# Optimization experiments

Hardware: AMD Instinct MI355X
Metric: run time of the kernel (lower is better)

The kernel has to match this reference:

```python
import jax, jax.numpy as jnp
import numpy as np

N_NODES = 100000
N_EDGES = 6400000
NODE_IN = 128
HID = 64


def _mlp(x, w1, b1, w2, b2):
    # Linear -> ReLU -> Linear -> ReLU
    return jax.nn.relu(jax.nn.relu(x @ w1 + b1) @ w2 + b2)


def _edge_softmax_agg(node_h, logits, src, dst, n):
    # DGL edge_softmax: softmax of edge logits over incoming edges per dst node,
    # then weighted sum of src node features scattered to dst.
    m = jax.lax.stop_gradient(jax.ops.segment_max(logits, dst, num_segments=n))
    e = jnp.exp(logits - m[dst])
    s = jax.ops.segment_sum(e, dst, num_segments=n)
    w = e / s[dst]
    return jax.ops.segment_sum(w * node_h[src], dst, num_segments=n)


def setup_inputs() -> dict:
    key = jax.random.key(0)
    ks = jax.random.split(key, 24)
    d = {
        "node_feat": jax.random.normal(ks[0], (N_NODES, NODE_IN), jnp.float32),
        "edge_feat": jax.random.normal(ks[1], (N_EDGES, 1), jnp.float32),
        "edge_dist": jax.random.normal(ks[2], (N_EDGES, 1), jnp.float32),
        "src": jax.random.randint(ks[3], (N_EDGES,), 0, N_NODES, jnp.int32),
        "dst": jax.random.randint(ks[4], (N_EDGES,), 0, N_NODES, jnp.int32),
    }
    def lin(k, fin, fout):
        kw, kb = jax.random.split(k)
        return (jax.random.normal(kw, (fin, fout), jnp.float32) / np.sqrt(fin),
                jax.random.normal(kb, (fout,), jnp.float32) * 0.01)
    d["enc_w1"], d["enc_b1"] = lin(ks[5], NODE_IN, HID)
    d["enc_w2"], d["enc_b2"] = lin(ks[6], HID, 1)
    d["nu_w1"], d["nu_b1"] = lin(ks[7], 2, HID)
    d["nu_w2"], d["nu_b2"] = lin(ks[8], HID, 1)
    d["eu_w1"], d["eu_b1"] = lin(ks[9], 3, HID)
    d["eu_w2"], d["eu_b2"] = lin(ks[10], HID, 1)
    d["dec_w1"], d["dec_b1"] = lin(ks[11], 1, HID)
    d["dec_w2"], d["dec_b2"] = lin(ks[12], HID, 1)
    return d


def reference(node_feat, edge_feat, edge_dist, src, dst,
              enc_w1, enc_b1, enc_w2, enc_b2,
              nu_w1, nu_b1, nu_w2, nu_b2,
              eu_w1, eu_b1, eu_w2, eu_b2,
              dec_w1, dec_b1, dec_w2, dec_b2):
    n = node_feat.shape[0]
    # encoder on raw node features -> [N,1]
    h = _mlp(node_feat, enc_w1, enc_b1, enc_w2, enc_b2)
    # softmax aggregation weighted by edge 'dist'
    h = _edge_softmax_agg(h, edge_dist, src, dst, n)
    # edge update: concat([edge_feat, src_h, dst_h]) -> MLP -> [E,1]
    eh = _mlp(jnp.concatenate([edge_feat, h[src], h[dst]], axis=-1),
              eu_w1, eu_b1, eu_w2, eu_b2)
    # pull: sum incoming updated edge features per dst node
    agg = jax.ops.segment_sum(eh, dst, num_segments=n)
    # node update: concat([agg_m, h]) -> MLP -> [N,1]
    h = _mlp(jnp.concatenate([agg, h], axis=-1), nu_w1, nu_b1, nu_w2, nu_b2)
    # second softmax aggregation with updated edge features as logits
    h2 = _edge_softmax_agg(h, eh, src, dst, n)
    # decoder -> [N,1]
    return _mlp(h2, dec_w1, dec_b1, dec_w2, dec_b2)
```

## Files before the change

### kernel.cpp

```cpp
#include <hip/hip_runtime.h>


#define NHB 256

typedef int   iv4 __attribute__((ext_vector_type(4)));
typedef float fv4 __attribute__((ext_vector_type(4)));
typedef float fv2 __attribute__((ext_vector_type(2)));

#if __has_builtin(__builtin_elementwise_fma)
#define FMA2(a, b, c) __builtin_elementwise_fma((a), (b), (c))
#else
static __device__ __forceinline__ fv2 FMA2(fv2 a, fv2 b, fv2 c) {
    fv2 r; r.x = fmaf(a.x, b.x, c.x); r.y = fmaf(a.y, b.y, c.y); return r;
}
#endif
#if __has_builtin(__builtin_elementwise_max)
#define MAX2(a, b) __builtin_elementwise_max((a), (b))
#else
static __device__ __forceinline__ fv2 MAX2(fv2 a, fv2 b) {
    fv2 r; r.x = fmaxf(a.x, b.x); r.y = fmaxf(a.y, b.y); return r;
}
#endif


__global__ void __launch_bounds__(1024) k_chist(
    const int* __restrict__ DST, int* __restrict__ hist,
    int e, int nbkt, int shift, int epb)
{
    __shared__ int lh[512];
    for (int c = threadIdx.x; c < nbkt; c += blockDim.x) lh[c] = 0;
    __syncthreads();
    int b = blockIdx.x;
    int i0 = b * epb, i1 = min(i0 + epb, e);
    int nq = (i1 > i0) ? ((i1 - i0) >> 2) : 0;
    const iv4* D4 = reinterpret_cast<const iv4*>(DST + i0);
    for (int q = threadIdx.x; q < nq; q += blockDim.x) {
        iv4 d = D4[q];
        atomicAdd(&lh[d.x >> shift], 1);
        atomicAdd(&lh[d.y >> shift], 1);
        atomicAdd(&lh[d.z >> shift], 1);
        atomicAdd(&lh[d.w >> shift], 1);
    }
    for (int i = i0 + 4 * nq + threadIdx.x; i < i1; i += blockDim.x)
        atomicAdd(&lh[DST[i] >> shift], 1);
    __syncthreads();
    for (int c = threadIdx.x; c < nbkt; c += blockDim.x)
        hist[(size_t)c * NHB + b] = lh[c];
}

__global__ void __launch_bounds__(256) k_scanA(
    int* __restrict__ hist, int* __restrict__ bktCnt)
{
    int c = blockIdx.x;
    int* row = hist + (size_t)c * NHB;
    __shared__ int part[256];
    int t = threadIdx.x;
    int v = row[t];
    part[t] = v;
    __syncthreads();
    for (int off = 1; off < 256; off <<= 1) {
        int x = 0;
        if (t >= off) x = part[t - off];
        __syncthreads();
        part[t] += x;
        __syncthreads();
    }
    if (t == 255) bktCnt[c] = part[255];
    row[t] = part[t] - v;
}

__global__ void __launch_bounds__(256) k_scanB(
    const int* __restrict__ bktCnt, int* __restrict__ base, int nbkt, int e)
{
    __shared__ int part[256];
    int t = threadIdx.x;
    int v[4];
    int sum = 0;
    #pragma unroll
    for (int u = 0; u < 4; ++u) {
        int idx = t * 4 + u;
        v[u] = (idx < nbkt) ? bktCnt[idx] : 0;
        sum += v[u];
    }
    part[t] = sum;
    __syncthreads();
    for (int off = 1; off < 256; off <<= 1) {
        int x = 0;
        if (t >= off) x = part[t - off];
        __syncthreads();
        part[t] += x;
        __syncthreads();
    }
    int run = (t == 0) ? 0 : part[t - 1];
    #pragma unroll
    for (int u = 0; u < 4; ++u) {
        int idx = t * 4 + u;
        if (idx < nbkt) base[idx] = run;
        run += v[u];
    }
    if (t == 0) base[nbkt] = e;
}

__global__ void __launch_bounds__(1024) k_scatter(
    const int* __restrict__ DST, const int* __restrict__ SRC,
    const float* __restrict__ DIST, const float* __restrict__ EF,
    const int* __restrict__ hist, const int* __restrict__ base,
    float2* __restrict__ payA, float* __restrict__ ef_s,
    int e, int nbkt, int shift, int epb)
{
    __shared__ int loff[512];
    int b = blockIdx.x;
    for (int c = threadIdx.x; c < nbkt; c += blockDim.x)
        loff[c] = base[c] + hist[(size_t)c * NHB + b];
    __syncthreads();
    int i0 = b * epb, i1 = min(i0 + epb, e);
    if (i0 >= i1) return;
    int mask = (1 << shift) - 1;
    int nq = (i1 - i0) >> 2;
    const iv4* D4 = reinterpret_cast<const iv4*>(DST + i0);
    const iv4* S4 = reinterpret_cast<const iv4*>(SRC + i0);
    const fv4* T4 = reinterpret_cast<const fv4*>(DIST + i0);
    const fv4* F4 = reinterpret_cast<const fv4*>(EF + i0);
    for (int q = threadIdx.x; q < nq; q += blockDim.x) {
        iv4 dv = __builtin_nontemporal_load(D4 + q);
        iv4 sv = __builtin_nontemporal_load(S4 + q);
        fv4 tv = __builtin_nontemporal_load(T4 + q);
        fv4 fv = __builtin_nontemporal_load(F4 + q);
        #pragma unroll
        for (int u = 0; u < 4; ++u) {
            int d = dv[u];
            int c = d >> shift;
            int pos = atomicAdd(&loff[c], 1);
            int sd = (sv[u] << shift) | (d & mask);
            payA[pos] = make_float2(__int_as_float(sd), tv[u]);
            ef_s[pos] = fv[u];
        }
    }
    for (int i = i0 + 4 * nq + threadIdx.x; i < i1; i += blockDim.x) {
        int d = DST[i];
        int c = d >> shift;
        int pos = atomicAdd(&loff[c], 1);
        int sd = (SRC[i] << shift) | (d & mask);
        payA[pos] = make_float2(__int_as_float(sd), DIST[i]);
        ef_s[pos] = EF[i];
    }
}


__global__ void __launch_bounds__(256) k_enc(
    const float* __restrict__ X, const float* __restrict__ W1,
    const float* __restrict__ B1, const float* __restrict__ W2,
    const float* __restrict__ B2, float* __restrict__ H0, int n)
{
    __shared__ float4 w1s[2048];
    for (int t = threadIdx.x; t < 2048; t += blockDim.x)
        w1s[t] = reinterpret_cast<const float4*>(W1)[t];
    __syncthreads();

    int i = blockIdx.x * blockDim.x + threadIdx.x;
    if (i >= n) return;

    const float4* xp = reinterpret_cast<const float4*>(X) + (size_t)i * 32;

    float acc[64];
    #pragma unroll
    for (int j = 0; j < 64; ++j) acc[j] = B1[j];

    for (int k4 = 0; k4 < 32; ++k4) {
        float4 xv = xp[k4];
        #pragma unroll
        for (int kk = 0; kk < 4; ++kk) {
            float x = (&xv.x)[kk];
            const float4* wrow = &w1s[(k4 * 4 + kk) * 16];
            #pragma unroll
            for (int j4 = 0; j4 < 16; ++j4) {
                float4 w = wrow[j4];
                acc[j4*4+0] = fmaf(x, w.x, acc[j4*4+0]);
                acc[j4*4+1] = fmaf(x, w.y, acc[j4*4+1]);
                acc[j4*4+2] = fmaf(x, w.z, acc[j4*4+2]);
                acc[j4*4+3] = fmaf(x, w.w, acc[j4*4+3]);
            }
        }
    }
    float o = B2[0];
    #pragma unroll
    for (int j = 0; j < 64; ++j)
        o = fmaf(fmaxf(acc[j], 0.f), W2[j], o);
    H0[i] = fmaxf(o, 0.f);
}


__global__ void __launch_bounds__(256) k_passA(
    const float2* __restrict__ payA, const float* __restrict__ H0,
    const int* __restrict__ base,
    float* __restrict__ pSum, float* __restrict__ pNum, int shift, int G)
{
    __shared__ float lsum[512], lnum[512];
    int c = blockIdx.x / G, g = blockIdx.x % G;
    int bw = 1 << shift, mask = bw - 1;
    for (int t = threadIdx.x; t < bw; t += blockDim.x) { lsum[t] = 0.f; lnum[t] = 0.f; }
    __syncthreads();
    int b0 = base[c], len = base[c + 1] - b0;
    int i0 = b0 + (int)(((long long)len * g) / G);
    int i1 = b0 + (int)(((long long)len * (g + 1)) / G);
    const int T = blockDim.x;
    for (int i = i0 + (int)threadIdx.x; i < i1; i += 4 * T) {
        fv2 p[4]; bool v[4]; int sd[4]; float h[4], ev[4];
        #pragma unroll
        for (int u = 0; u < 4; ++u) {
            int j = i + u * T;
            v[u] = j < i1;
            p[u] = (fv2){0.f, 0.f};
            if (v[u]) p[u] = __builtin_nontemporal_load(
                          reinterpret_cast<const fv2*>(payA) + j);
        }
        #pragma unroll
        for (int u = 0; u < 4; ++u) {
            sd[u] = __float_as_int(p[u].x);
            h[u] = v[u] ? H0[sd[u] >> shift] : 0.f;
        }
        #pragma unroll
        for (int u = 0; u < 4; ++u) ev[u] = __expf(p[u].y);
        #pragma unroll
        for (int u = 0; u < 4; ++u) {
            if (v[u]) {
                atomicAdd(&lsum[sd[u] & mask], ev[u]);
                atomicAdd(&lnum[sd[u] & mask], ev[u] * h[u]);
            }
        }
    }
    __syncthreads();
    size_t po = (size_t)blockIdx.x << shift;
    for (int t = threadIdx.x; t < bw; t += blockDim.x) {
        pSum[po + t] = lsum[t];
        pNum[po + t] = lnum[t];
    }
}

__global__ void __launch_bounds__(256) k_finA(
    const float* __restrict__ pSum, const float* __restrict__ pNum,
    float* __restrict__ H1, int shift, int n, int G)
{
    int d = blockIdx.x * blockDim.x + threadIdx.x;
    if (d >= n) return;
    int c = d >> shift, t = d & ((1 << shift) - 1);
    size_t b = (size_t)c * G << shift;
    int bw = 1 << shift;
    float s = 0.f, m = 0.f;
    for (int g = 0; g < G; ++g) {
        s += pSum[b + (size_t)g * bw + t];
        m += pNum[b + (size_t)g * bw + t];
    }
    H1[d] = (s != 0.f) ? m / s : 0.f;
}

__global__ void __launch_bounds__(256) k_passB(
    const float2* __restrict__ payA, float* __restrict__ ef_s,
    const float* __restrict__ H1,
    const float* __restrict__ W1, const float* __restrict__ B1,
    const float* __restrict__ W2, const float* __restrict__ B2,
    const int* __restrict__ base,
    float* __restrict__ pAgg, float* __restrict__ pS2, int shift, int n, int G)
{
    __shared__ float lagg[512], ls2[512];
    const fv2 ZERO2 = {0.f, 0.f};
    int bw = 1 << shift, mask = bw - 1;
    int c = blockIdx.x / G, g = blockIdx.x % G;
    int d0 = c << shift;
    for (int t = threadIdx.x; t < bw; t += blockDim.x) {
        lagg[t] = 0.f;
        ls2[t] = 0.f;
    }
    __syncthreads();
    const float b2 = B2[0];
    int b0 = base[c], len = base[c + 1] - b0;
    int i0 = b0 + (int)(((long long)len * g) / G);
    int i1 = b0 + (int)(((long long)len * (g + 1)) / G);
    const int T = blockDim.x;
    const int STEP = 4 * T;

    int i = i0 + (int)threadIdx.x;

    fv2 pa[4]; float xa[4];
    fv2 pb[4]; float xb[4];
    float hsc[4], hdc[4];
    #pragma unroll
    for (int u = 0; u < 4; ++u) {
        int j = i + u * T;
        pa[u] = ZERO2; xa[u] = 0.f;
        if (j < i1) {
            pa[u] = __builtin_nontemporal_load(
                reinterpret_cast<const fv2*>(payA) + j);
            xa[u] = __builtin_nontemporal_load(ef_s + j);
        }
    }
    #pragma unroll
    for (int u = 0; u < 4; ++u) {
        int j = i + STEP + u * T;
        pb[u] = ZERO2; xb[u] = 0.f;
        if (j < i1) {
            pb[u] = __builtin_nontemporal_load(
                reinterpret_cast<const fv2*>(payA) + j);
            xb[u] = __builtin_nontemporal_load(ef_s + j);
        }
    }
    #pragma unroll
    for (int u = 0; u < 4; ++u) {
        int sd = __float_as_int(pa[u].x);
        hsc[u] = H1[sd >> shift];
        hdc[u] = H1[d0 + (sd & mask)];
    }

    while (i < i1) {
        int i2 = i + 2 * STEP;
        fv2 pc[4]; float xc[4];
        #pragma unroll
        for (int u = 0; u < 4; ++u) {
            int j = i2 + u * T;
            pc[u] = ZERO2; xc[u] = 0.f;
            if (j < i1) {
                pc[u] = __builtin_nontemporal_load(
                    reinterpret_cast<const fv2*>(payA) + j);
                xc[u] = __builtin_nontemporal_load(ef_s + j);
            }
        }
        float hsn[4], hdn[4];
        #pragma unroll
        for (int u = 0; u < 4; ++u) {
            int sd = __float_as_int(pb[u].x);
            hsn[u] = H1[sd >> shift];
            hdn[u] = H1[d0 + (sd & mask)];
        }
        fv2 x0v[4], hsv[4], hdv[4], o2[4];
        int lo[4];
        #pragma unroll
        for (int u = 0; u < 4; ++u) {
            lo[u] = __float_as_int(pa[u].x) & mask;
            fv2 xt; xt.x = xa[u]; xt.y = xa[u];
            x0v[u] = xt;
            fv2 ht; ht.x = hsc[u]; ht.y = hsc[u];
            hsv[u] = ht;
            fv2 dt; dt.x = hdc[u]; dt.y = hdc[u];
            hdv[u] = dt;
            o2[u] = ZERO2;
        }
        #pragma unroll 4
        for (int j = 0; j < 64; j += 2) {
            fv2 aj = *reinterpret_cast<const fv2*>(W1 + j);
            fv2 bj = *reinterpret_cast<const fv2*>(W1 + 64 + j);
            fv2 cj = *reinterpret_cast<const fv2*>(W1 + 128 + j);
            fv2 dj = *reinterpret_cast<const fv2*>(B1 + j);
            fv2 vj = *reinterpret_cast<const fv2*>(W2 + j);
            #pragma unroll
            for (int u = 0; u < 4; ++u) {
                fv2 t = FMA2(x0v[u], aj,
                         FMA2(hsv[u], bj, FMA2(hdv[u], cj, dj)));
                t = MAX2(t, ZERO2);
                o2[u] = FMA2(t, vj, o2[u]);
            }
        }
        #pragma unroll
        for (int u = 0; u < 4; ++u) {
            int j = i + u * T;
            if (j < i1) {
                float eh = fmaxf(o2[u].x + o2[u].y + b2, 0.f);
                float ex = __expf(eh);
                ef_s[j] = ex;
                atomicAdd(&lagg[lo[u]], eh);
                atomicAdd(&ls2[lo[u]], ex);
            }
        }
        i += STEP;
        #pragma unroll
        for (int u = 0; u < 4; ++u) {
            pa[u] = pb[u]; xa[u] = xb[u];
            pb[u] = pc[u]; xb[u] = xc[u];
            hsc[u] = hsn[u]; hdc[u] = hdn[u];
        }
    }
    __syncthreads();
    size_t po = (size_t)blockIdx.x << shift;
    for (int t = threadIdx.x; t < bw; t += blockDim.x) {
        pAgg[po + t] = lagg[t];
        pS2[po + t] = ls2[t];
    }
}

__global__ void __launch_bounds__(256) k_finB(
    const float* __restrict__ pAgg, const float* __restrict__ pS2,
    const float* __restrict__ H1,
    const float* __restrict__ NW1, const float* __restrict__ NB1,
    const float* __restrict__ NW2, const float* __restrict__ NB2,
    float* __restrict__ H2, float* __restrict__ S2, int shift, int n, int G)
{
    int d = blockIdx.x * blockDim.x + threadIdx.x;
    if (d >= n) return;
    int c = d >> shift, t = d & ((1 << shift) - 1);
    size_t b = (size_t)c * G << shift;
    int bw = 1 << shift;
    float agg = 0.f, s2 = 0.f;
    for (int g = 0; g < G; ++g) {
        agg += pAgg[b + (size_t)g * bw + t];
        s2  += pS2[b + (size_t)g * bw + t];
    }
    float xh = H1[d];
    float o = NB2[0];
    #pragma unroll 4
    for (int j = 0; j < 64; ++j) {
        float a = fmaf(agg, NW1[j], fmaf(xh, NW1[64 + j], NB1[j]));
        o = fmaf(fmaxf(a, 0.f), NW2[j], o);
    }
    H2[d] = fmaxf(o, 0.f);
    S2[d] = s2;
}

__global__ void __launch_bounds__(256) k_passC(
    const float2* __restrict__ payA, const float* __restrict__ e2_s,
    const float* __restrict__ H2, const int* __restrict__ base,
    float* __restrict__ pNum, int shift, int G)
{
    __shared__ float lnum[512];
    int c = blockIdx.x / G, g = blockIdx.x % G;
    int bw = 1 << shift, mask = bw - 1;
    for (int t = threadIdx.x; t < bw; t += blockDim.x) lnum[t] = 0.f;
    __syncthreads();
    int b0 = base[c], len = base[c + 1] - b0;
    int i0 = b0 + (int)(((long long)len * g) / G);
    int i1 = b0 + (int)(((long long)len * (g + 1)) / G);
    const int T = blockDim.x;
    for (int i = i0 + (int)threadIdx.x; i < i1; i += 4 * T) {
        fv2 p[4]; float e2[4]; bool v[4]; int sd[4]; float h[4];
        #pragma unroll
        for (int u = 0; u < 4; ++u) {
            int j = i + u * T;
            v[u] = j < i1;
            p[u] = (fv2){0.f, 0.f}; e2[u] = 0.f;
            if (v[u]) {
                p[u] = __builtin_nontemporal_load(
                    reinterpret_cast<const fv2*>(payA) + j);
                e2[u] = __builtin_nontemporal_load(e2_s + j);
            }
        }
        #pragma unroll
        for (int u = 0; u < 4; ++u) {
            sd[u] = __float_as_int(p[u].x);
            h[u] = v[u] ? H2[sd[u] >> shift] : 0.f;
        }
        #pragma unroll
        for (int u = 0; u < 4; ++u) {
            if (v[u]) atomicAdd(&lnum[sd[u] & mask], e2[u] * h[u]);
        }
    }
    __syncthreads();
    size_t po = (size_t)blockIdx.x << shift;
    for (int t = threadIdx.x; t < bw; t += blockDim.x)
        pNum[po + t] = lnum[t];
}

__global__ void __launch_bounds__(256) k_finC(
    const float* __restrict__ pNum, const float* __restrict__ S2,
    const float* __restrict__ W1, const float* __restrict__ B1,
    const float* __restrict__ W2, const float* __restrict__ B2,
    float* __restrict__ OUT, int shift, int n, int G)
{
    int d = blockIdx.x * blockDim.x + threadIdx.x;
    if (d >= n) return;
    int c = d >> shift, t = d & ((1 << shift) - 1);
    size_t b = (size_t)c * G << shift;
    int bw = 1 << shift;
    float m = 0.f;
    for (int g = 0; g < G; ++g) m += pNum[b + (size_t)g * bw + t];
    float s = S2[d];
    float x = (s != 0.f) ? m / s : 0.f;
    float o = B2[0];
    #pragma unroll 4
    for (int j = 0; j < 64; ++j) {
        float a = fmaf(x, W1[j], B1[j]);
        o = fmaf(fmaxf(a, 0.f), W2[j], o);
    }
    OUT[d] = fmaxf(o, 0.f);
}


__device__ __forceinline__ void atomAddF(float* p, float v) { unsafeAtomicAdd(p, v); }

__global__ void k_zero(float* __restrict__ p, int n) {
    int i = blockIdx.x * blockDim.x + threadIdx.x;
    if (i < n) p[i] = 0.f;
}

__global__ void __launch_bounds__(256) k_agg1(
    const float* __restrict__ DIST, const int* __restrict__ SRC,
    const int* __restrict__ DST, const float* __restrict__ H0,
    float* __restrict__ S1, float* __restrict__ NUM1, int e)
{
    int i = blockIdx.x * blockDim.x + threadIdx.x;
    if (i >= e) return;
    float ev = __expf(DIST[i]);
    atomAddF(&S1[DST[i]], ev);
    atomAddF(&NUM1[DST[i]], ev * H0[SRC[i]]);
}

__global__ void k_div(const float* __restrict__ NUM, const float* __restrict__ S,
                      float* __restrict__ H, int n) {
    int i = blockIdx.x * blockDim.x + threadIdx.x;
    if (i < n) {
        float s = S[i];
        H[i] = (s != 0.f) ? NUM[i] / s : 0.f;
    }
}

__global__ void __launch_bounds__(256) k_edgeF(
    const float* __restrict__ EF, const int* __restrict__ SRC,
    const int* __restrict__ DST, const float* __restrict__ H1,
    const float* __restrict__ W1, const float* __restrict__ B1,
    const float* __restrict__ W2, const float* __restrict__ B2,
    float* __restrict__ E2, float* __restrict__ AGG, float* __restrict__ S2, int e)
{
    int i = blockIdx.x * blockDim.x + threadIdx.x;
    if (i >= e) return;
    float x0 = EF[i];
    int s = SRC[i], d = DST[i];
    float h_s = H1[s], h_d = H1[d];
    float o = B2[0];
    for (int j = 0; j < 64; ++j) {
        float aj = fmaf(x0, W1[j], fmaf(h_s, W1[64+j], fmaf(h_d, W1[128+j], B1[j])));
        o = fmaf(fmaxf(aj, 0.f), W2[j], o);
    }
    float eh = fmaxf(o, 0.f);
    float ex = __expf(eh);
    E2[i] = ex;
    atomAddF(&AGG[d], eh);
    atomAddF(&S2[d], ex);
}

__global__ void k_nu(const float* __restrict__ AGG, const float* __restrict__ H1,
                     const float* __restrict__ W1, const float* __restrict__ B1,
                     const float* __restrict__ W2, const float* __restrict__ B2,
                     float* __restrict__ H2, int n)
{
    int i = blockIdx.x * blockDim.x + threadIdx.x;
    if (i >= n) return;
    float x0 = AGG[i], x1 = H1[i];
    float o = B2[0];
    #pragma unroll
    for (int j = 0; j < 64; ++j) {
        float a = fmaf(x0, W1[j], fmaf(x1, W1[64 + j], B1[j]));
        o = fmaf(fmaxf(a, 0.f), W2[j], o);
    }
    H2[i] = fmaxf(o, 0.f);
}

__global__ void __launch_bounds__(256) k_agg2F(
    const float* __restrict__ E2, const int* __restrict__ SRC,
    const int* __restrict__ DST, const float* __restrict__ H2,
    float* __restrict__ NUM2, int e)
{
    int i = blockIdx.x * blockDim.x + threadIdx.x;
    if (i >= e) return;
    atomAddF(&NUM2[DST[i]], E2[i] * H2[SRC[i]]);
}

__global__ void k_final(const float* __restrict__ NUM2, const float* __restrict__ S2,
                        const float* __restrict__ W1, const float* __restrict__ B1,
                        const float* __restrict__ W2, const float* __restrict__ B2,
                        float* __restrict__ OUT, int n)
{
    int i = blockIdx.x * blockDim.x + threadIdx.x;
    if (i >= n) return;
    float s = S2[i];
    float x = (s != 0.f) ? NUM2[i] / s : 0.f;
    float o = B2[0];
    #pragma unroll
    for (int j = 0; j < 64; ++j) {
        float a = fmaf(x, W1[j], B1[j]);
        o = fmaf(fmaxf(a, 0.f), W2[j], o);
    }
    OUT[i] = fmaxf(o, 0.f);
}


extern "C" void kernel_launch(void* const* d_in, const int* in_sizes, int n_in,
                              void* d_out, int out_size, void* d_ws, size_t ws_size,
                              hipStream_t stream)
{
    const float* node_feat = (const float*)d_in[0];
    const float* edge_feat = (const float*)d_in[1];
    const float* edge_dist = (const float*)d_in[2];
    const int*   src       = (const int*)d_in[3];
    const int*   dst       = (const int*)d_in[4];
    const float* enc_w1 = (const float*)d_in[5];
    const float* enc_b1 = (const float*)d_in[6];
    const float* enc_w2 = (const float*)d_in[7];
    const float* enc_b2 = (const float*)d_in[8];
    const float* nu_w1  = (const float*)d_in[9];
    const float* nu_b1  = (const float*)d_in[10];
    const float* nu_w2  = (const float*)d_in[11];
    const float* nu_b2  = (const float*)d_in[12];
    const float* eu_w1  = (const float*)d_in[13];
    const float* eu_b1  = (const float*)d_in[14];
    const float* eu_w2  = (const float*)d_in[15];
    const float* eu_b2  = (const float*)d_in[16];
    const float* dec_w1 = (const float*)d_in[17];
    const float* dec_b1 = (const float*)d_in[18];
    const float* dec_w2 = (const float*)d_in[19];
    const float* dec_b2 = (const float*)d_in[20];

    const int n = in_sizes[0] / 128;
    const int e = in_sizes[1];
    const int B = 256;

    int shift = 9;
    while ((((n + (1 << shift) - 1) >> shift) > 512) && shift < 12) shift++;
    const int nbkt = (n + (1 << shift) - 1) >> shift;
    int epb = (e + NHB - 1) / NHB;
    epb = (epb + 3) & ~3;

    float* ws = (float*)d_ws;
    size_t w = (size_t)4 * n;
    int* base   = (int*)(ws + w); w += nbkt + 1;
    int* bktCnt = (int*)(ws + w); w += nbkt;
    int* hist   = (int*)(ws + w); w += (size_t)nbkt * NHB;
    w = (w + 1) & ~(size_t)1;
    float2* payA = (float2*)(ws + w); w += (size_t)2 * e;
    float* ef_s  = ws + w; w += e;

    int G = 16;
    size_t psz;
    size_t need;
    for (;;) {
        psz = ((size_t)nbkt * G) << shift;
        need = (w + 2 * psz) * 4;
        if (need <= ws_size || G == 1) break;
        G >>= 1;
    }
    float* pP0 = ws + w;
    float* pP1 = ws + w + psz;

    float* h0 = ws;
    float* h1 = ws + (size_t)1 * n;
    float* h2 = ws + (size_t)2 * n;
    float* s2 = ws + (size_t)3 * n;

    if (ws_size >= need && nbkt <= 512 && (1 << shift) <= 512 &&
        ((size_t)n << shift) < (1u << 30)) {
        const int gE = nbkt * G;
        hipLaunchKernelGGL(k_chist, dim3(NHB), dim3(1024), 0, stream,
                           dst, hist, e, nbkt, shift, epb);
        hipLaunchKernelGGL(k_scanA, dim3(nbkt), dim3(B), 0, stream, hist, bktCnt);
        hipLaunchKernelGGL(k_scanB, dim3(1), dim3(B), 0, stream, bktCnt, base, nbkt, e);
        hipLaunchKernelGGL(k_scatter, dim3(NHB), dim3(1024), 0, stream,
                           dst, src, edge_dist, edge_feat, hist, base,
                           payA, ef_s, e, nbkt, shift, epb);
        hipLaunchKernelGGL(k_enc, dim3((n + B - 1) / B), dim3(B), 0, stream,
                           node_feat, enc_w1, enc_b1, enc_w2, enc_b2, h0, n);
        hipLaunchKernelGGL(k_passA, dim3(gE), dim3(B), 0, stream,
                           payA, h0, base, pP0, pP1, shift, G);
        hipLaunchKernelGGL(k_finA, dim3((n + B - 1) / B), dim3(B), 0, stream,
                           pP0, pP1, h1, shift, n, G);
        hipLaunchKernelGGL(k_passB, dim3(gE), dim3(B), 0, stream,
                           payA, ef_s, h1, eu_w1, eu_b1, eu_w2, eu_b2, base,
                           pP0, pP1, shift, n, G);
        hipLaunchKernelGGL(k_finB, dim3((n + B - 1) / B), dim3(B), 0, stream,
                           pP0, pP1, h1, nu_w1, nu_b1, nu_w2, nu_b2, h2, s2,
                           shift, n, G);
        hipLaunchKernelGGL(k_passC, dim3(gE), dim3(B), 0, stream,
                           payA, ef_s , h2, base, pP0, shift, G);
        hipLaunchKernelGGL(k_finC, dim3((n + B - 1) / B), dim3(B), 0, stream,
                           pP0, s2, dec_w1, dec_b1, dec_w2, dec_b2,
                           (float*)d_out, shift, n, G);
    } else {
        float* agg  = ws + (size_t)2 * n;
        float* s1   = ws + (size_t)4 * n;
        float* num1 = ws + (size_t)5 * n;
        float* num2 = ws + (size_t)6 * n;
        float* h2f  = ws + (size_t)7 * n;
        float* e2   = ws + (size_t)8 * n;
        hipLaunchKernelGGL(k_zero, dim3((5 * n + B - 1) / B), dim3(B), 0, stream,
                           agg, 5 * n);
        hipLaunchKernelGGL(k_enc, dim3((n + B - 1) / B), dim3(B), 0, stream,
                           node_feat, enc_w1, enc_b1, enc_w2, enc_b2, h0, n);
        hipLaunchKernelGGL(k_agg1, dim3((e + B - 1) / B), dim3(B), 0, stream,
                           edge_dist, src, dst, h0, s1, num1, e);
        hipLaunchKernelGGL(k_div, dim3((n + B - 1) / B), dim3(B), 0, stream,
                           num1, s1, h1, n);
        hipLaunchKernelGGL(k_edgeF, dim3((e + B - 1) / B), dim3(B), 0, stream,
                           edge_feat, src, dst, h1, eu_w1, eu_b1, eu_w2, eu_b2,
                           e2, agg, s2, e);
        hipLaunchKernelGGL(k_nu, dim3((n + B - 1) / B), dim3(B), 0, stream,
                           agg, h1, nu_w1, nu_b1, nu_w2, nu_b2, h2f, n);
        hipLaunchKernelGGL(k_agg2F, dim3((e + B - 1) / B), dim3(B), 0, stream,
                           e2, src, dst, h2f, num2, e);
        hipLaunchKernelGGL(k_final, dim3((n + B - 1) / B), dim3(B), 0, stream,
                           num2, s2, dec_w1, dec_b1, dec_w2, dec_b2, (float*)d_out, n);
    }
}
```

Before: 392.3 us.

## Store edge exp into payload slot, cache dst h1 in LDS, simplify prefetch

k_passB now writes exp(eh) into the dist half of the packed payload instead of a separate ef_s array. k_passC then reads a single float2 stream rather than payload plus ef_s, which removes one separate read stream from passC. Destination-node h1 values for the bucket are staged in shared memory, and the prefetch depth drops from two steps to one with the src gather done inline. The payload is overwritten in place, so later passes cannot see the original dist, and the shallower prefetch may expose more gather latency.

```diff
diff --git a/kernel.cpp b/kernel.cpp
--- a/kernel.cpp
+++ b/kernel.cpp
@@ -210,7 +210,7 @@
         for (int u = 0; u < 4; ++u) {
             int j = i + u * T;
             v[u] = j < i1;
-            p[u] = (fv2){0.f, 0.f};
+            p[u].x = 0.f; p[u].y = 0.f;
             if (v[u]) p[u] = __builtin_nontemporal_load(
                           reinterpret_cast<const fv2*>(payA) + j);
         }
@@ -255,19 +255,21 @@
 }
 
 __global__ void __launch_bounds__(256) k_passB(
-    const float2* __restrict__ payA, float* __restrict__ ef_s,
+    float2* __restrict__ payA, const float* __restrict__ ef_s,
     const float* __restrict__ H1,
     const float* __restrict__ W1, const float* __restrict__ B1,
     const float* __restrict__ W2, const float* __restrict__ B2,
     const int* __restrict__ base,
     float* __restrict__ pAgg, float* __restrict__ pS2, int shift, int n, int G)
 {
-    __shared__ float lagg[512], ls2[512];
+    __shared__ float h1loc[512], lagg[512], ls2[512];
     const fv2 ZERO2 = {0.f, 0.f};
     int bw = 1 << shift, mask = bw - 1;
     int c = blockIdx.x / G, g = blockIdx.x % G;
     int d0 = c << shift;
     for (int t = threadIdx.x; t < bw; t += blockDim.x) {
+        int d = d0 + t;
+        h1loc[t] = (d < n) ? H1[d] : 0.f;
         lagg[t] = 0.f;
         ls2[t] = 0.f;
     }
@@ -277,70 +279,46 @@
     int i0 = b0 + (int)(((long long)len * g) / G);
     int i1 = b0 + (int)(((long long)len * (g + 1)) / G);
     const int T = blockDim.x;
-    const int STEP = 4 * T;
 
     int i = i0 + (int)threadIdx.x;
-
-    fv2 pa[4]; float xa[4];
-    fv2 pb[4]; float xb[4];
-    float hsc[4], hdc[4];
+    fv2 pa[4]; float xf[4];
     #pragma unroll
     for (int u = 0; u < 4; ++u) {
         int j = i + u * T;
-        pa[u] = ZERO2; xa[u] = 0.f;
+        pa[u] = ZERO2; xf[u] = 0.f;
         if (j < i1) {
             pa[u] = __builtin_nontemporal_load(
                 reinterpret_cast<const fv2*>(payA) + j);
-            xa[u] = __builtin_nontemporal_load(ef_s + j);
-        }
-    }
-    #pragma unroll
-    for (int u = 0; u < 4; ++u) {
-        int j = i + STEP + u * T;
-        pb[u] = ZERO2; xb[u] = 0.f;
-        if (j < i1) {
-            pb[u] = __builtin_nontemporal_load(
-                reinterpret_cast<const fv2*>(payA) + j);
-            xb[u] = __builtin_nontemporal_load(ef_s + j);
-        }
-    }
-    #pragma unroll
-    for (int u = 0; u < 4; ++u) {
-        int sd = __float_as_int(pa[u].x);
-        hsc[u] = H1[sd >> shift];
-        hdc[u] = H1[d0 + (sd & mask)];
-    }
-
+            xf[u] = __builtin_nontemporal_load(ef_s + j);
+        }
+    }
+    float* payF = reinterpret_cast<float*>(payA);
     while (i < i1) {
-        int i2 = i + 2 * STEP;
-        fv2 pc[4]; float xc[4];
-        #pragma unroll
-        for (int u = 0; u < 4; ++u) {
-            int j = i2 + u * T;
-            pc[u] = ZERO2; xc[u] = 0.f;
+        int inext = i + 4 * T;
+        fv2 pb[4]; float xg[4];
+        #pragma unroll
+        for (int u = 0; u < 4; ++u) {
+            int j = inext + u * T;
+            pb[u] = ZERO2; xg[u] = 0.f;
             if (j < i1) {
-                pc[u] = __builtin_nontemporal_load(
+                pb[u] = __builtin_nontemporal_load(
                     reinterpret_cast<const fv2*>(payA) + j);
-                xc[u] = __builtin_nontemporal_load(ef_s + j);
+                xg[u] = __builtin_nontemporal_load(ef_s + j);
             }
-        }
-        float hsn[4], hdn[4];
-        #pragma unroll
-        for (int u = 0; u < 4; ++u) {
-            int sd = __float_as_int(pb[u].x);
-            hsn[u] = H1[sd >> shift];
-            hdn[u] = H1[d0 + (sd & mask)];
         }
         fv2 x0v[4], hsv[4], hdv[4], o2[4];
         int lo[4];
         #pragma unroll
         for (int u = 0; u < 4; ++u) {
-            lo[u] = __float_as_int(pa[u].x) & mask;
-            fv2 xt; xt.x = xa[u]; xt.y = xa[u];
+            int sd = __float_as_int(pa[u].x);
+            lo[u] = sd & mask;
+            float hs = H1[sd >> shift];
+            float hd = h1loc[lo[u]];
+            fv2 xt; xt.x = xf[u]; xt.y = xf[u];
             x0v[u] = xt;
-            fv2 ht; ht.x = hsc[u]; ht.y = hsc[u];
+            fv2 ht; ht.x = hs; ht.y = hs;
             hsv[u] = ht;
-            fv2 dt; dt.x = hdc[u]; dt.y = hdc[u];
+            fv2 dt; dt.x = hd; dt.y = hd;
             hdv[u] = dt;
             o2[u] = ZERO2;
         }
@@ -365,18 +343,14 @@
             if (j < i1) {
                 float eh = fmaxf(o2[u].x + o2[u].y + b2, 0.f);
                 float ex = __expf(eh);
-                ef_s[j] = ex;
+                payF[2 * j + 1] = ex;
                 atomicAdd(&lagg[lo[u]], eh);
                 atomicAdd(&ls2[lo[u]], ex);
             }
         }
-        i += STEP;
-        #pragma unroll
-        for (int u = 0; u < 4; ++u) {
-            pa[u] = pb[u]; xa[u] = xb[u];
-            pb[u] = pc[u]; xb[u] = xc[u];
-            hsc[u] = hsn[u]; hdc[u] = hdn[u];
-        }
+        i = inext;
+        #pragma unroll
+        for (int u = 0; u < 4; ++u) { pa[u] = pb[u]; xf[u] = xg[u]; }
     }
     __syncthreads();
     size_t po = (size_t)blockIdx.x << shift;
@@ -415,7 +389,7 @@
 }
 
 __global__ void __launch_bounds__(256) k_passC(
-    const float2* __restrict__ payA, const float* __restrict__ e2_s,
+    const float2* __restrict__ payA,
     const float* __restrict__ H2, const int* __restrict__ base,
     float* __restrict__ pNum, int shift, int G)
 {
@@ -429,17 +403,14 @@
     int i1 = b0 + (int)(((long long)len * (g + 1)) / G);
     const int T = blockDim.x;
     for (int i = i0 + (int)threadIdx.x; i < i1; i += 4 * T) {
-        fv2 p[4]; float e2[4]; bool v[4]; int sd[4]; float h[4];
+        fv2 p[4]; bool v[4]; int sd[4]; float h[4];
         #pragma unroll
         for (int u = 0; u < 4; ++u) {
             int j = i + u * T;
             v[u] = j < i1;
-            p[u] = (fv2){0.f, 0.f}; e2[u] = 0.f;
-            if (v[u]) {
-                p[u] = __builtin_nontemporal_load(
-                    reinterpret_cast<const fv2*>(payA) + j);
-                e2[u] = __builtin_nontemporal_load(e2_s + j);
-            }
+            p[u].x = 0.f; p[u].y = 0.f;
+            if (v[u]) p[u] = __builtin_nontemporal_load(
+                          reinterpret_cast<const fv2*>(payA) + j);
         }
         #pragma unroll
         for (int u = 0; u < 4; ++u) {
@@ -448,7 +419,7 @@
         }
         #pragma unroll
         for (int u = 0; u < 4; ++u) {
-            if (v[u]) atomicAdd(&lnum[sd[u] & mask], e2[u] * h[u]);
+            if (v[u]) atomicAdd(&lnum[sd[u] & mask], p[u].y * h[u]);
         }
     }
     __syncthreads();
@@ -665,7 +636,7 @@
                            pP0, pP1, h1, nu_w1, nu_b1, nu_w2, nu_b2, h2, s2,
                            shift, n, G);
         hipLaunchKernelGGL(k_passC, dim3(gE), dim3(B), 0, stream,
-                           payA, ef_s , h2, base, pP0, shift, G);
+                           payA, h2, base, pP0, shift, G);
         hipLaunchKernelGGL(k_finC, dim3((n + B - 1) / B), dim3(B), 0, stream,
                            pP0, s2, dec_w1, dec_b1, dec_w2, dec_b2,
                            (float*)d_out, shift, n, G);
```

Result: faster. 377.7 us (-3.7%).
